# Kernel optimization log

Hardware: AMD Instinct MI355X
Metric: run time of the kernel (lower is better)

Reference implementation:

```python
import jax, jax.numpy as jnp
import numpy as np

N = 100000   # nodes
E = 1200000  # edges
IN, HID, OUT = 64, 64, 64
G = 64       # graphs in the batch


def setup_inputs() -> dict:
    key = jax.random.key(0)
    ks = jax.random.split(key, 7)
    x = jax.random.normal(ks[0], (N, IN), dtype=jnp.float32)
    edge_index = jax.random.randint(ks[1], (2, E), 0, N, dtype=jnp.int32)
    batch = jnp.sort(jax.random.randint(ks[2], (N,), 0, G, dtype=jnp.int32))
    W1 = jax.random.normal(ks[3], (IN, HID), dtype=jnp.float32) * (1.0 / np.sqrt(IN))
    b1 = jnp.zeros((HID,), dtype=jnp.float32)
    W2 = jax.random.normal(ks[4], (HID, OUT), dtype=jnp.float32) * (1.0 / np.sqrt(HID))
    b2 = jnp.zeros((OUT,), dtype=jnp.float32)
    return {"x": x, "edge_index": edge_index, "batch": batch,
            "W1": W1, "b1": b1, "W2": W2, "b2": b2}


def _gcn_conv(x, W, b, src, dst, dinv):
    # x' = D^{-1/2} (A + I) D^{-1/2} (x W) + b   (PyG GCNConv with self-loops)
    h = x @ W                                   # [N, F_out]
    norm = dinv[src] * dinv[dst]                # [E]
    agg = jax.ops.segment_sum(h[src] * norm[:, None], dst, num_segments=N)
    agg = agg + h * (dinv * dinv)[:, None]      # self-loop contribution
    return agg + b


def reference(x, edge_index, batch, W1, b1, W2, b2):
    src, dst = edge_index[0], edge_index[1]
    # degree with self-loops, counted at the aggregation target (PyG convention)
    deg = jax.ops.segment_sum(jnp.ones((E,), x.dtype), dst, num_segments=N) + 1.0
    dinv = jax.lax.rsqrt(deg)

    h1 = jax.nn.relu(_gcn_conv(x, W1, b1, src, dst, dinv))   # [N, HID]
    s1 = jax.ops.segment_sum(h1, batch, num_segments=G)      # [G, HID]
    h2 = jax.nn.relu(_gcn_conv(h1, W2, b2, src, dst, dinv))  # [N, OUT]
    s2 = jax.ops.segment_sum(h2, batch, num_segments=G)      # [G, OUT]
    return h2, jnp.concatenate([s1, s2], axis=1)
```

## Files before the change

kernel.cpp:

```cpp
#include <hip/hip_runtime.h>


#define FDIM 64
#define BSHIFT 7
#define MAXNB 1024
#define EBCAP 2048
#define COLCAP 3072
#define BCAP 4096

__device__ __forceinline__ unsigned short f2bf(float f) {
    union { float f; unsigned int u; } a; a.f = f;
    unsigned int u = a.u;
    unsigned int r = u + 0x7fffu + ((u >> 16) & 1u);
    return (unsigned short)(r >> 16);
}
__device__ __forceinline__ float bf2f(unsigned short s) {
    union { unsigned int u; float f; } a; a.u = ((unsigned int)s) << 16;
    return a.f;
}

__global__ __launch_bounds__(256, 4) void k_pre(
    const int* __restrict__ src, const int* __restrict__ dstp, int E,
    const int* __restrict__ batch, int N, int G, int gemmB, int scatB,
    const float* __restrict__ x, const float* __restrict__ W1,
    int* __restrict__ bucketFill, int* __restrict__ gstart,
    unsigned short* __restrict__ gb1, unsigned int* __restrict__ ebuf) {
    __shared__ __align__(16) char sm[33792];
    int tid = threadIdx.x;
    int bx = blockIdx.x;
    if (bx < gemmB) {
        float4* Ws = (float4*)sm;
        float (*Xs)[68] = (float(*)[68])(sm + 16384);
        ushort4* GB4 = (ushort4*)gb1;
        if (bx == 0 && tid < 16) GB4[(size_t)N * 16 + tid] = make_ushort4(0, 0, 0, 0);
        const float4* W4 = (const float4*)W1;
        for (int i = tid; i < 1024; i += 256) Ws[i] = W4[i];
        int rowBase = bx * 64;
        for (int i = tid; i < 1024; i += 256) {
            int r = i >> 4, f4 = i & 15;
            float4 v = make_float4(0.f, 0.f, 0.f, 0.f);
            if (rowBase + r < N) v = ((const float4*)x)[(size_t)(rowBase + r) * 16 + f4];
            *(float4*)&Xs[r][f4 * 4] = v;
        }
        __syncthreads();
        int r0 = (tid >> 4) * 4;
        int c4 = tid & 15;
        float4 acc0 = make_float4(0,0,0,0), acc1 = acc0, acc2 = acc0, acc3 = acc0;
#pragma unroll 16
        for (int k = 0; k < 64; k++) {
            float4 w = Ws[k * 16 + c4];
            float x0 = Xs[r0 + 0][k], x1 = Xs[r0 + 1][k], x2 = Xs[r0 + 2][k], x3 = Xs[r0 + 3][k];
            acc0.x += x0 * w.x; acc0.y += x0 * w.y; acc0.z += x0 * w.z; acc0.w += x0 * w.w;
            acc1.x += x1 * w.x; acc1.y += x1 * w.y; acc1.z += x1 * w.z; acc1.w += x1 * w.w;
            acc2.x += x2 * w.x; acc2.y += x2 * w.y; acc2.z += x2 * w.z; acc2.w += x2 * w.w;
            acc3.x += x3 * w.x; acc3.y += x3 * w.y; acc3.z += x3 * w.z; acc3.w += x3 * w.w;
        }
        float4 a[4] = {acc0, acc1, acc2, acc3};
#pragma unroll
        for (int i = 0; i < 4; i++) {
            int row = rowBase + r0 + i;
            if (row < N) {
                ushort4 pk;
                pk.x = f2bf(a[i].x); pk.y = f2bf(a[i].y);
                pk.z = f2bf(a[i].z); pk.w = f2bf(a[i].w);
                GB4[(size_t)row * 16 + c4] = pk;
            }
        }
        return;
    }
    if (bx < gemmB + scatB) {
        int* hist = (int*)sm;
        int* base = hist + MAXNB;
        for (int i = tid; i < MAXNB; i += 256) hist[i] = 0;
        __syncthreads();
        int e0 = (bx - gemmB) * 4096;
        int s[16], d[16], r[16];
#pragma unroll
        for (int k = 0; k < 16; k++) {
            int e = e0 + k * 256 + tid;
            bool valid = e < E;
            s[k] = valid ? src[e] : 0;
            d[k] = valid ? dstp[e] : 0;
            r[k] = valid ? atomicAdd(&hist[d[k] >> BSHIFT], 1) : 0;
        }
        __syncthreads();
        for (int i = tid; i < MAXNB; i += 256) {
            int c = hist[i];
            base[i] = c ? (i << 11) + atomicAdd(&bucketFill[i], c) : 0;
        }
        __syncthreads();
#pragma unroll
        for (int k = 0; k < 16; k++) {
            int e = e0 + k * 256 + tid;
            if (e < E)
                ebuf[base[d[k] >> BSHIFT] + r[k]] =
                    (unsigned int)s[k] | ((unsigned int)(d[k] & 127) << 17);
        }
        return;
    }
    int i = (bx - gemmB - scatB) * 256 + tid;
    if (i < N) {
        int b = batch[i];
        if (i == 0) { for (int g = 0; g <= b; g++) gstart[g] = 0; }
        else {
            int pp = batch[i - 1];
            for (int g = pp + 1; g <= b; g++) gstart[g] = i;
        }
        if (i == N - 1) { for (int g = b + 1; g <= G; g++) gstart[g] = N; }
    }
}

__global__ __launch_bounds__(256) void k_bsort(const unsigned int* __restrict__ ebuf,
                                               const int* __restrict__ bucketFill, int N,
                                               int* __restrict__ row_ptr,
                                               int* __restrict__ row_blocks,
                                               int* __restrict__ col,
                                               float* __restrict__ dinv,
                                               unsigned short* __restrict__ gb1) {
    __shared__ int cntL[128];
    __shared__ int scanL[128];
    __shared__ int fillL[128];
    __shared__ int colL[BCAP];
    __shared__ int padT;
    int b = blockIdx.x;
    int n0 = b << BSHIFT;
    int nCnt = N - n0; if (nCnt > 128) nCnt = 128;
    int t = threadIdx.x;
    if (b == 0 && t == 0) dinv[N] = 0.f;
    int cnt = bucketFill[b]; if (cnt > EBCAP) cnt = EBCAP;
    int lo = b << 11, hi = lo + cnt;
    int outBase = b * COLCAP;
    if (t < 128) { cntL[t] = 0; fillL[t] = 0; }
    __syncthreads();
    for (int e = lo + t; e < hi; e += 256)
        atomicAdd(&cntL[ebuf[e] >> 17], 1);
    __syncthreads();
    int pc = 0;
    if (t < 128) { pc = (cntL[t] + 7) & ~7; scanL[t] = pc; }
    __syncthreads();
    for (int off = 1; off < 128; off <<= 1) {
        int u = (t >= off && t < 128) ? scanL[t - off] : 0;
        __syncthreads();
        if (t < 128) scanL[t] += u;
        __syncthreads();
    }
    if (t == 127) padT = scanL[127];
    if (t < nCnt) {
        int ex = scanL[t] - pc;
        row_ptr[n0 + t] = outBase + ex;
        row_blocks[n0 + t] = pc >> 3;
        dinv[n0 + t] = rsqrtf((float)cntL[t] + 1.0f);
        scanL[t] = ex;
    }
    __syncthreads();
    int padTotal = padT;
    if (padTotal <= BCAP) {
        for (int i = t; i < padTotal; i += 256) colL[i] = N;
        __syncthreads();
        for (int e = lo + t; e < hi; e += 256) {
            unsigned int pr = ebuf[e];
            int d = pr >> 17;
            int r = scanL[d] + atomicAdd(&fillL[d], 1);
            colL[r] = (int)(pr & 0x1FFFFu);
        }
        __syncthreads();
        for (int i = t; i < padTotal; i += 256) col[outBase + i] = colL[i];
    } else {
        for (int e = lo + t; e < hi; e += 256) {
            unsigned int pr = ebuf[e];
            int d = pr >> 17;
            int r = scanL[d] + atomicAdd(&fillL[d], 1);
            col[outBase + r] = (int)(pr & 0x1FFFFu);
        }
        __syncthreads();
        if (t < nCnt) {
            int pcl = (cntL[t] + 7) & ~7;
            for (int i = cntL[t]; i < pcl; i++) col[outBase + scanL[t] + i] = N;
        }
    }
    __syncthreads();
    ushort4* GB4 = (ushort4*)gb1;
    for (int i = t; i < nCnt * 16; i += 256) {
        int row = i >> 4, u4 = i & 15;
        float dn = rsqrtf((float)cntL[row] + 1.0f);
        size_t idx = (size_t)(n0 + row) * 16 + u4;
        ushort4 u = GB4[idx];
        u.x = f2bf(bf2f(u.x) * dn);
        u.y = f2bf(bf2f(u.y) * dn);
        u.z = f2bf(bf2f(u.z) * dn);
        u.w = f2bf(bf2f(u.w) * dn);
        GB4[idx] = u;
    }
}

template <typename OutT>
__global__ __launch_bounds__(256) void k_agg(
    const unsigned short* __restrict__ Gb,
    const int* __restrict__ row_ptr, const int* __restrict__ row_blocks,
    const int* __restrict__ col, const float* __restrict__ dinv,
    const float* __restrict__ bias, int N, OutT* __restrict__ Out) {
    int w = threadIdx.x >> 6;
    int c = threadIdx.x & 63;
    int n = blockIdx.x * 4 + w;
    if (n >= N) return;
    int e = row_ptr[n];
    int nb8 = row_blocks[n];
    float acc = bf2f(Gb[(size_t)n * FDIM + c]);
    for (; nb8 >= 2; nb8 -= 2, e += 16) {
        int4 ca = *(const int4*)(col + e);
        int4 cb = *(const int4*)(col + e + 4);
        int4 cc = *(const int4*)(col + e + 8);
        int4 cd = *(const int4*)(col + e + 12);
        int s0  = __builtin_amdgcn_readfirstlane(ca.x);
        int s1  = __builtin_amdgcn_readfirstlane(ca.y);
        int s2  = __builtin_amdgcn_readfirstlane(ca.z);
        int s3  = __builtin_amdgcn_readfirstlane(ca.w);
        int s4  = __builtin_amdgcn_readfirstlane(cb.x);
        int s5  = __builtin_amdgcn_readfirstlane(cb.y);
        int s6  = __builtin_amdgcn_readfirstlane(cb.z);
        int s7  = __builtin_amdgcn_readfirstlane(cb.w);
        int s8  = __builtin_amdgcn_readfirstlane(cc.x);
        int s9  = __builtin_amdgcn_readfirstlane(cc.y);
        int s10 = __builtin_amdgcn_readfirstlane(cc.z);
        int s11 = __builtin_amdgcn_readfirstlane(cc.w);
        int s12 = __builtin_amdgcn_readfirstlane(cd.x);
        int s13 = __builtin_amdgcn_readfirstlane(cd.y);
        int s14 = __builtin_amdgcn_readfirstlane(cd.z);
        int s15 = __builtin_amdgcn_readfirstlane(cd.w);
        float a0  = bf2f(Gb[(size_t)s0  * FDIM + c]);
        float a1  = bf2f(Gb[(size_t)s1  * FDIM + c]);
        float a2  = bf2f(Gb[(size_t)s2  * FDIM + c]);
        float a3  = bf2f(Gb[(size_t)s3  * FDIM + c]);
        float a4  = bf2f(Gb[(size_t)s4  * FDIM + c]);
        float a5  = bf2f(Gb[(size_t)s5  * FDIM + c]);
        float a6  = bf2f(Gb[(size_t)s6  * FDIM + c]);
        float a7  = bf2f(Gb[(size_t)s7  * FDIM + c]);
        float a8  = bf2f(Gb[(size_t)s8  * FDIM + c]);
        float a9  = bf2f(Gb[(size_t)s9  * FDIM + c]);
        float a10 = bf2f(Gb[(size_t)s10 * FDIM + c]);
        float a11 = bf2f(Gb[(size_t)s11 * FDIM + c]);
        float a12 = bf2f(Gb[(size_t)s12 * FDIM + c]);
        float a13 = bf2f(Gb[(size_t)s13 * FDIM + c]);
        float a14 = bf2f(Gb[(size_t)s14 * FDIM + c]);
        float a15 = bf2f(Gb[(size_t)s15 * FDIM + c]);
        acc += (((a0 + a1) + (a2 + a3)) + ((a4 + a5) + (a6 + a7)))
             + (((a8 + a9) + (a10 + a11)) + ((a12 + a13) + (a14 + a15)));
    }
    if (nb8) {
        int4 ca = *(const int4*)(col + e);
        int4 cb = *(const int4*)(col + e + 4);
        int s0 = __builtin_amdgcn_readfirstlane(ca.x);
        int s1 = __builtin_amdgcn_readfirstlane(ca.y);
        int s2 = __builtin_amdgcn_readfirstlane(ca.z);
        int s3 = __builtin_amdgcn_readfirstlane(ca.w);
        int s4 = __builtin_amdgcn_readfirstlane(cb.x);
        int s5 = __builtin_amdgcn_readfirstlane(cb.y);
        int s6 = __builtin_amdgcn_readfirstlane(cb.z);
        int s7 = __builtin_amdgcn_readfirstlane(cb.w);
        float a0 = bf2f(Gb[(size_t)s0 * FDIM + c]);
        float a1 = bf2f(Gb[(size_t)s1 * FDIM + c]);
        float a2 = bf2f(Gb[(size_t)s2 * FDIM + c]);
        float a3 = bf2f(Gb[(size_t)s3 * FDIM + c]);
        float a4 = bf2f(Gb[(size_t)s4 * FDIM + c]);
        float a5 = bf2f(Gb[(size_t)s5 * FDIM + c]);
        float a6 = bf2f(Gb[(size_t)s6 * FDIM + c]);
        float a7 = bf2f(Gb[(size_t)s7 * FDIM + c]);
        acc += ((a0 + a1) + (a2 + a3)) + ((a4 + a5) + (a6 + a7));
    }
    float v = fmaxf(acc * dinv[n] + bias[c], 0.f);
    if constexpr (sizeof(OutT) == 2)
        Out[(size_t)n * FDIM + c] = f2bf(v);
    else
        Out[(size_t)n * FDIM + c] = v;
}

__global__ __launch_bounds__(256, 4) void k_gemm2(
    const unsigned short* __restrict__ H1b, const float* __restrict__ W2,
    const float* __restrict__ dinv, int N, unsigned short* __restrict__ Gb2) {
    __shared__ float4 Ws[64 * 16];
    __shared__ float Xs[64][68];
    int tid = threadIdx.x;
    ushort4* GB4 = (ushort4*)Gb2;
    if (blockIdx.x == 0 && tid < 16)
        GB4[(size_t)N * 16 + tid] = make_ushort4(0, 0, 0, 0);
    const float4* W4 = (const float4*)W2;
    for (int i = tid; i < 1024; i += 256) Ws[i] = W4[i];
    int rowBase = blockIdx.x * 64;
    const ushort4* H4 = (const ushort4*)H1b;
    for (int i = tid; i < 1024; i += 256) {
        int r = i >> 4, u4 = i & 15;
        float4 v = make_float4(0.f, 0.f, 0.f, 0.f);
        if (rowBase + r < N) {
            ushort4 u = H4[(size_t)(rowBase + r) * 16 + u4];
            v = make_float4(bf2f(u.x), bf2f(u.y), bf2f(u.z), bf2f(u.w));
        }
        *(float4*)&Xs[r][u4 * 4] = v;
    }
    __syncthreads();
    int r0 = (tid >> 4) * 4;
    int c4 = tid & 15;
    float4 acc0 = make_float4(0,0,0,0), acc1 = acc0, acc2 = acc0, acc3 = acc0;
#pragma unroll 16
    for (int k = 0; k < 64; k++) {
        float4 w = Ws[k * 16 + c4];
        float x0 = Xs[r0 + 0][k], x1 = Xs[r0 + 1][k], x2 = Xs[r0 + 2][k], x3 = Xs[r0 + 3][k];
        acc0.x += x0 * w.x; acc0.y += x0 * w.y; acc0.z += x0 * w.z; acc0.w += x0 * w.w;
        acc1.x += x1 * w.x; acc1.y += x1 * w.y; acc1.z += x1 * w.z; acc1.w += x1 * w.w;
        acc2.x += x2 * w.x; acc2.y += x2 * w.y; acc2.z += x2 * w.z; acc2.w += x2 * w.w;
        acc3.x += x3 * w.x; acc3.y += x3 * w.y; acc3.z += x3 * w.z; acc3.w += x3 * w.w;
    }
    float4 a[4] = {acc0, acc1, acc2, acc3};
#pragma unroll
    for (int i = 0; i < 4; i++) {
        int row = rowBase + r0 + i;
        if (row < N) {
            float dn = dinv[row];
            ushort4 pk;
            pk.x = f2bf(a[i].x * dn);
            pk.y = f2bf(a[i].y * dn);
            pk.z = f2bf(a[i].z * dn);
            pk.w = f2bf(a[i].w * dn);
            GB4[(size_t)row * 16 + c4] = pk;
        }
    }
}

__global__ __launch_bounds__(256) void k_pool(const unsigned short* __restrict__ H1b,
                                              const float4* __restrict__ H2,
                                              const int* __restrict__ gstart,
                                              float* __restrict__ pool) {
    int g = blockIdx.x & 63;
    int layer = blockIdx.x >> 6;
    int lo = gstart[g], hi = gstart[g + 1];
    int c4 = threadIdx.x & 15;
    int rl = threadIdx.x >> 4;
    float4 acc = make_float4(0.f, 0.f, 0.f, 0.f);
    if (layer == 0) {
        const ushort4* H = (const ushort4*)H1b;
        for (int r = lo + rl; r < hi; r += 16) {
            ushort4 u = H[(size_t)r * 16 + c4];
            acc.x += bf2f(u.x); acc.y += bf2f(u.y);
            acc.z += bf2f(u.z); acc.w += bf2f(u.w);
        }
    } else {
        for (int r = lo + rl; r < hi; r += 16) {
            float4 v = H2[(size_t)r * 16 + c4];
            acc.x += v.x; acc.y += v.y; acc.z += v.z; acc.w += v.w;
        }
    }
    __shared__ float4 sm[16][16];
    sm[rl][c4] = acc;
    __syncthreads();
    if (rl == 0) {
        float4 s = sm[0][c4];
#pragma unroll
        for (int k = 1; k < 16; k++) {
            float4 v = sm[k][c4];
            s.x += v.x; s.y += v.y; s.z += v.z; s.w += v.w;
        }
        float* dstq = &pool[(size_t)g * 128 + layer * 64 + c4 * 4];
        dstq[0] = s.x; dstq[1] = s.y; dstq[2] = s.z; dstq[3] = s.w;
    }
}

static inline size_t align256(size_t x) { return (x + 255) & ~(size_t)255; }

extern "C" void kernel_launch(void* const* d_in, const int* in_sizes, int n_in,
                              void* d_out, int out_size, void* d_ws, size_t ws_size,
                              hipStream_t stream) {
    const float* x     = (const float*)d_in[0];
    const int*   ei    = (const int*)d_in[1];
    const int*   batch = (const int*)d_in[2];
    const float* W1    = (const float*)d_in[3];
    const float* b1    = (const float*)d_in[4];
    const float* W2    = (const float*)d_in[5];
    const float* b2    = (const float*)d_in[6];

    const int N = in_sizes[0] / FDIM;
    const int E = in_sizes[1] / 2;
    const int G = 64;
    const int NB = (N + 127) >> BSHIFT;
    const int* src = ei;
    const int* dst = ei + E;

    char* p = (char*)d_ws;
    int* row_ptr     = (int*)p; p += align256(((size_t)N + 1) * 4);
    int* row_blocks  = (int*)p; p += align256((size_t)N * 4);
    int* col         = (int*)p; p += align256((size_t)NB * COLCAP * 4);
    int* bucketFill  = (int*)p; p += align256((size_t)MAXNB * 4);
    int* gstart      = (int*)p; p += align256((size_t)(G + 1) * 4);
    float* dinv      = (float*)p; p += align256(((size_t)N + 1) * 4);
    unsigned short* gb1 = (unsigned short*)p; p += align256(((size_t)N + 1) * FDIM * 2);
    unsigned short* gb2 = (unsigned short*)p; p += align256(((size_t)N + 1) * FDIM * 2);
    unsigned short* h1b = (unsigned short*)p; p += align256((size_t)N * FDIM * 2);
    unsigned int* ebuf = (unsigned int*)h1b;

    float* out  = (float*)d_out;
    float* h2   = out;
    float* pool = out + (size_t)N * FDIM;

    hipMemsetAsync(bucketFill, 0, (size_t)MAXNB * 4, stream);

    int nbB   = (N + 255) / 256;
    int gemmB = (N + 63) / 64;
    int aggB  = (N + 3) / 4;
    int scatB = (E + 4095) / 4096;

    k_pre<<<gemmB + scatB + nbB, 256, 0, stream>>>(src, dst, E, batch, N, G,
                                                   gemmB, scatB, x, W1,
                                                   bucketFill, gstart, gb1, ebuf);
    k_bsort<<<NB, 256, 0, stream>>>(ebuf, bucketFill, N, row_ptr, row_blocks,
                                    col, dinv, gb1);
    k_agg<unsigned short><<<aggB, 256, 0, stream>>>(gb1, row_ptr, row_blocks, col,
                                                    dinv, b1, N, h1b);
    k_gemm2<<<gemmB, 256, 0, stream>>>(h1b, W2, dinv, N, gb2);
    k_agg<float><<<aggB, 256, 0, stream>>>(gb2, row_ptr, row_blocks, col,
                                           dinv, b2, N, h2);
    k_pool<<<2 * G, 256, 0, stream>>>(h1b, (const float4*)h2, gstart, pool);
}
```

Before: 244.2 us.

## Fuse graph pooling into gemm2 and agg2, move dinv scaling into agg1

Removes the separate pooling kernel and the gstart computation. Layer-1 pooling now runs inside k_gemm2 over its staged H1 tile, and layer-2 pooling runs inside the second aggregation, both with per-graph running sums and atomicAdd after zeroing pool with a memset. The pass in k_bsort that rescaled gb1 by dinv is dropped. Instead the first aggregation multiplies each gathered neighbour by dinv[src], which adds 16 scalar gathers per edge block in exchange for one fewer read-modify-write of gb1. It adds atomic traffic and a block-level sync in the aggregation kernel.

```diff
diff --git a/kernel.cpp b/kernel.cpp
--- a/kernel.cpp
+++ b/kernel.cpp
@@ -21,9 +21,9 @@
 
 __global__ __launch_bounds__(256, 4) void k_pre(
     const int* __restrict__ src, const int* __restrict__ dstp, int E,
-    const int* __restrict__ batch, int N, int G, int gemmB, int scatB,
+    int N, int gemmB,
     const float* __restrict__ x, const float* __restrict__ W1,
-    int* __restrict__ bucketFill, int* __restrict__ gstart,
+    int* __restrict__ bucketFill,
     unsigned short* __restrict__ gb1, unsigned int* __restrict__ ebuf) {
     __shared__ __align__(16) char sm[33792];
     int tid = threadIdx.x;
@@ -68,45 +68,32 @@
         }
         return;
     }
-    if (bx < gemmB + scatB) {
-        int* hist = (int*)sm;
-        int* base = hist + MAXNB;
-        for (int i = tid; i < MAXNB; i += 256) hist[i] = 0;
-        __syncthreads();
-        int e0 = (bx - gemmB) * 4096;
-        int s[16], d[16], r[16];
+    int* hist = (int*)sm;
+    int* base = hist + MAXNB;
+    for (int i = tid; i < MAXNB; i += 256) hist[i] = 0;
+    __syncthreads();
+    int e0 = (bx - gemmB) * 4096;
+    int s[16], d[16], r[16];
 #pragma unroll
-        for (int k = 0; k < 16; k++) {
-            int e = e0 + k * 256 + tid;
-            bool valid = e < E;
-            s[k] = valid ? src[e] : 0;
-            d[k] = valid ? dstp[e] : 0;
-            r[k] = valid ? atomicAdd(&hist[d[k] >> BSHIFT], 1) : 0;
-        }
-        __syncthreads();
-        for (int i = tid; i < MAXNB; i += 256) {
-            int c = hist[i];
-            base[i] = c ? (i << 11) + atomicAdd(&bucketFill[i], c) : 0;
-        }
-        __syncthreads();
+    for (int k = 0; k < 16; k++) {
+        int e = e0 + k * 256 + tid;
+        bool valid = e < E;
+        s[k] = valid ? src[e] : 0;
+        d[k] = valid ? dstp[e] : 0;
+        r[k] = valid ? atomicAdd(&hist[d[k] >> BSHIFT], 1) : 0;
+    }
+    __syncthreads();
+    for (int i = tid; i < MAXNB; i += 256) {
+        int c = hist[i];
+        base[i] = c ? (i << 11) + atomicAdd(&bucketFill[i], c) : 0;
+    }
+    __syncthreads();
 #pragma unroll
-        for (int k = 0; k < 16; k++) {
-            int e = e0 + k * 256 + tid;
-            if (e < E)
-                ebuf[base[d[k] >> BSHIFT] + r[k]] =
-                    (unsigned int)s[k] | ((unsigned int)(d[k] & 127) << 17);
-        }
-        return;
-    }
-    int i = (bx - gemmB - scatB) * 256 + tid;
-    if (i < N) {
-        int b = batch[i];
-        if (i == 0) { for (int g = 0; g <= b; g++) gstart[g] = 0; }
-        else {
-            int pp = batch[i - 1];
-            for (int g = pp + 1; g <= b; g++) gstart[g] = i;
-        }
-        if (i == N - 1) { for (int g = b + 1; g <= G; g++) gstart[g] = N; }
+    for (int k = 0; k < 16; k++) {
+        int e = e0 + k * 256 + tid;
+        if (e < E)
+            ebuf[base[d[k] >> BSHIFT] + r[k]] =
+                (unsigned int)s[k] | ((unsigned int)(d[k] & 127) << 17);
     }
 }
 
@@ -115,8 +102,7 @@
                                                int* __restrict__ row_ptr,
                                                int* __restrict__ row_blocks,
                                                int* __restrict__ col,
-                                               float* __restrict__ dinv,
-                                               unsigned short* __restrict__ gb1) {
+                                               float* __restrict__ dinv) {
     __shared__ int cntL[128];
     __shared__ int scanL[128];
     __shared__ int fillL[128];
@@ -178,34 +164,28 @@
             for (int i = cntL[t]; i < pcl; i++) col[outBase + scanL[t] + i] = N;
         }
     }
-    __syncthreads();
-    ushort4* GB4 = (ushort4*)gb1;
-    for (int i = t; i < nCnt * 16; i += 256) {
-        int row = i >> 4, u4 = i & 15;
-        float dn = rsqrtf((float)cntL[row] + 1.0f);
-        size_t idx = (size_t)(n0 + row) * 16 + u4;
-        ushort4 u = GB4[idx];
-        u.x = f2bf(bf2f(u.x) * dn);
-        u.y = f2bf(bf2f(u.y) * dn);
-        u.z = f2bf(bf2f(u.z) * dn);
-        u.w = f2bf(bf2f(u.w) * dn);
-        GB4[idx] = u;
-    }
-}
-
-template <typename OutT>
+}
+
+template <typename OutT, bool EDGE_DINV, bool POOL>
 __global__ __launch_bounds__(256) void k_agg(
     const unsigned short* __restrict__ Gb,
     const int* __restrict__ row_ptr, const int* __restrict__ row_blocks,
     const int* __restrict__ col, const float* __restrict__ dinv,
-    const float* __restrict__ bias, int N, OutT* __restrict__ Out) {
+    const float* __restrict__ bias, const int* __restrict__ batch,
+    int N, OutT* __restrict__ Out, float* __restrict__ pool) {
     int w = threadIdx.x >> 6;
     int c = threadIdx.x & 63;
     int n = blockIdx.x * 4 + w;
-    if (n >= N) return;
-    int e = row_ptr[n];
-    int nb8 = row_blocks[n];
-    float acc = bf2f(Gb[(size_t)n * FDIM + c]);
+    bool alive = n < N;
+    int e = 0, nb8 = 0;
+    float acc = 0.f, dn = 0.f;
+    if (alive) {
+        e = row_ptr[n];
+        nb8 = row_blocks[n];
+        dn = dinv[n];
+        float self = bf2f(Gb[(size_t)n * FDIM + c]);
+        acc = EDGE_DINV ? self * dn : self;
+    }
     for (; nb8 >= 2; nb8 -= 2, e += 16) {
         int4 ca = *(const int4*)(col + e);
         int4 cb = *(const int4*)(col + e + 4);
@@ -243,8 +223,17 @@
         float a13 = bf2f(Gb[(size_t)s13 * FDIM + c]);
         float a14 = bf2f(Gb[(size_t)s14 * FDIM + c]);
         float a15 = bf2f(Gb[(size_t)s15 * FDIM + c]);
-        acc += (((a0 + a1) + (a2 + a3)) + ((a4 + a5) + (a6 + a7)))
-             + (((a8 + a9) + (a10 + a11)) + ((a12 + a13) + (a14 + a15)));
+        if constexpr (EDGE_DINV) {
+            float d0  = dinv[s0],  d1  = dinv[s1],  d2  = dinv[s2],  d3  = dinv[s3];
+            float d4  = dinv[s4],  d5  = dinv[s5],  d6  = dinv[s6],  d7  = dinv[s7];
+            float d8  = dinv[s8],  d9  = dinv[s9],  d10 = dinv[s10], d11 = dinv[s11];
+            float d12 = dinv[s12], d13 = dinv[s13], d14 = dinv[s14], d15 = dinv[s15];
+            acc += (((a0*d0 + a1*d1) + (a2*d2 + a3*d3)) + ((a4*d4 + a5*d5) + (a6*d6 + a7*d7)))
+                 + (((a8*d8 + a9*d9) + (a10*d10 + a11*d11)) + ((a12*d12 + a13*d13) + (a14*d14 + a15*d15)));
+        } else {
+            acc += (((a0 + a1) + (a2 + a3)) + ((a4 + a5) + (a6 + a7)))
+                 + (((a8 + a9) + (a10 + a11)) + ((a12 + a13) + (a14 + a15)));
+        }
     }
     if (nb8) {
         int4 ca = *(const int4*)(col + e);
@@ -265,20 +254,51 @@
         float a5 = bf2f(Gb[(size_t)s5 * FDIM + c]);
         float a6 = bf2f(Gb[(size_t)s6 * FDIM + c]);
         float a7 = bf2f(Gb[(size_t)s7 * FDIM + c]);
-        acc += ((a0 + a1) + (a2 + a3)) + ((a4 + a5) + (a6 + a7));
-    }
-    float v = fmaxf(acc * dinv[n] + bias[c], 0.f);
-    if constexpr (sizeof(OutT) == 2)
-        Out[(size_t)n * FDIM + c] = f2bf(v);
-    else
-        Out[(size_t)n * FDIM + c] = v;
+        if constexpr (EDGE_DINV) {
+            float d0 = dinv[s0], d1 = dinv[s1], d2 = dinv[s2], d3 = dinv[s3];
+            float d4 = dinv[s4], d5 = dinv[s5], d6 = dinv[s6], d7 = dinv[s7];
+            acc += ((a0*d0 + a1*d1) + (a2*d2 + a3*d3)) + ((a4*d4 + a5*d5) + (a6*d6 + a7*d7));
+        } else {
+            acc += ((a0 + a1) + (a2 + a3)) + ((a4 + a5) + (a6 + a7));
+        }
+    }
+    float v = 0.f;
+    if (alive) {
+        v = fmaxf(acc * dn + bias[c], 0.f);
+        if constexpr (sizeof(OutT) == 2)
+            Out[(size_t)n * FDIM + c] = f2bf(v);
+        else
+            Out[(size_t)n * FDIM + c] = v;
+    }
+    if constexpr (POOL) {
+        __shared__ float smv[4][64];
+        __shared__ int gsm[4];
+        smv[w][c] = v;
+        if (c == 0) gsm[w] = alive ? batch[n] : -1;
+        __syncthreads();
+        if (w == 0) {
+            float run = 0.f; int gcur = -2;
+#pragma unroll
+            for (int i = 0; i < 4; i++) {
+                int g = gsm[i];
+                if (g != gcur) {
+                    if (gcur >= 0) atomicAdd(&pool[(size_t)gcur * 128 + 64 + c], run);
+                    run = 0.f; gcur = g;
+                }
+                run += smv[i][c];
+            }
+            if (gcur >= 0) atomicAdd(&pool[(size_t)gcur * 128 + 64 + c], run);
+        }
+    }
 }
 
 __global__ __launch_bounds__(256, 4) void k_gemm2(
     const unsigned short* __restrict__ H1b, const float* __restrict__ W2,
-    const float* __restrict__ dinv, int N, unsigned short* __restrict__ Gb2) {
+    const float* __restrict__ dinv, const int* __restrict__ batch, int N,
+    unsigned short* __restrict__ Gb2, float* __restrict__ pool) {
     __shared__ float4 Ws[64 * 16];
     __shared__ float Xs[64][68];
+    __shared__ int bsL[64];
     int tid = threadIdx.x;
     ushort4* GB4 = (ushort4*)Gb2;
     if (blockIdx.x == 0 && tid < 16)
@@ -286,6 +306,10 @@
     const float4* W4 = (const float4*)W2;
     for (int i = tid; i < 1024; i += 256) Ws[i] = W4[i];
     int rowBase = blockIdx.x * 64;
+    if (tid < 64) {
+        int row = rowBase + tid;
+        bsL[tid] = (row < N) ? batch[row] : -1;
+    }
     const ushort4* H4 = (const ushort4*)H1b;
     for (int i = tid; i < 1024; i += 256) {
         int r = i >> 4, u4 = i & 15;
@@ -323,43 +347,21 @@
             GB4[(size_t)row * 16 + c4] = pk;
         }
     }
-}
-
-__global__ __launch_bounds__(256) void k_pool(const unsigned short* __restrict__ H1b,
-                                              const float4* __restrict__ H2,
-                                              const int* __restrict__ gstart,
-                                              float* __restrict__ pool) {
-    int g = blockIdx.x & 63;
-    int layer = blockIdx.x >> 6;
-    int lo = gstart[g], hi = gstart[g + 1];
-    int c4 = threadIdx.x & 15;
-    int rl = threadIdx.x >> 4;
-    float4 acc = make_float4(0.f, 0.f, 0.f, 0.f);
-    if (layer == 0) {
-        const ushort4* H = (const ushort4*)H1b;
-        for (int r = lo + rl; r < hi; r += 16) {
-            ushort4 u = H[(size_t)r * 16 + c4];
-            acc.x += bf2f(u.x); acc.y += bf2f(u.y);
-            acc.z += bf2f(u.z); acc.w += bf2f(u.w);
-        }
-    } else {
-        for (int r = lo + rl; r < hi; r += 16) {
-            float4 v = H2[(size_t)r * 16 + c4];
-            acc.x += v.x; acc.y += v.y; acc.z += v.z; acc.w += v.w;
-        }
-    }
-    __shared__ float4 sm[16][16];
-    sm[rl][c4] = acc;
-    __syncthreads();
-    if (rl == 0) {
-        float4 s = sm[0][c4];
-#pragma unroll
-        for (int k = 1; k < 16; k++) {
-            float4 v = sm[k][c4];
-            s.x += v.x; s.y += v.y; s.z += v.z; s.w += v.w;
-        }
-        float* dstq = &pool[(size_t)g * 128 + layer * 64 + c4 * 4];
-        dstq[0] = s.x; dstq[1] = s.y; dstq[2] = s.z; dstq[3] = s.w;
+    {
+        int cc = tid & 63;
+        int seg = tid >> 6;
+        float run = 0.f; int gcur = -2;
+        for (int rl = 0; rl < 16; rl++) {
+            int r = seg * 16 + rl;
+            int g = bsL[r];
+            if (g < 0) break;
+            if (g != gcur) {
+                if (gcur >= 0) atomicAdd(&pool[(size_t)gcur * 128 + cc], run);
+                run = 0.f; gcur = g;
+            }
+            run += Xs[r][cc];
+        }
+        if (gcur >= 0) atomicAdd(&pool[(size_t)gcur * 128 + cc], run);
     }
 }
 
@@ -388,7 +390,6 @@
     int* row_blocks  = (int*)p; p += align256((size_t)N * 4);
     int* col         = (int*)p; p += align256((size_t)NB * COLCAP * 4);
     int* bucketFill  = (int*)p; p += align256((size_t)MAXNB * 4);
-    int* gstart      = (int*)p; p += align256((size_t)(G + 1) * 4);
     float* dinv      = (float*)p; p += align256(((size_t)N + 1) * 4);
     unsigned short* gb1 = (unsigned short*)p; p += align256(((size_t)N + 1) * FDIM * 2);
     unsigned short* gb2 = (unsigned short*)p; p += align256(((size_t)N + 1) * FDIM * 2);
@@ -400,21 +401,19 @@
     float* pool = out + (size_t)N * FDIM;
 
     hipMemsetAsync(bucketFill, 0, (size_t)MAXNB * 4, stream);
-
-    int nbB   = (N + 255) / 256;
+    hipMemsetAsync(pool, 0, (size_t)G * 128 * 4, stream);
+
     int gemmB = (N + 63) / 64;
     int aggB  = (N + 3) / 4;
     int scatB = (E + 4095) / 4096;
 
-    k_pre<<<gemmB + scatB + nbB, 256, 0, stream>>>(src, dst, E, batch, N, G,
-                                                   gemmB, scatB, x, W1,
-                                                   bucketFill, gstart, gb1, ebuf);
+    k_pre<<<gemmB + scatB, 256, 0, stream>>>(src, dst, E, N, gemmB, x, W1,
+                                             bucketFill, gb1, ebuf);
     k_bsort<<<NB, 256, 0, stream>>>(ebuf, bucketFill, N, row_ptr, row_blocks,
-                                    col, dinv, gb1);
-    k_agg<unsigned short><<<aggB, 256, 0, stream>>>(gb1, row_ptr, row_blocks, col,
-                                                    dinv, b1, N, h1b);
-    k_gemm2<<<gemmB, 256, 0, stream>>>(h1b, W2, dinv, N, gb2);
-    k_agg<float><<<aggB, 256, 0, stream>>>(gb2, row_ptr, row_blocks, col,
-                                           dinv, b2, N, h2);
-    k_pool<<<2 * G, 256, 0, stream>>>(h1b, (const float4*)h2, gstart, pool);
-}
+                                    col, dinv);
+    k_agg<unsigned short, true, false><<<aggB, 256, 0, stream>>>(
+        gb1, row_ptr, row_blocks, col, dinv, b1, nullptr, N, h1b, nullptr);
+    k_gemm2<<<gemmB, 256, 0, stream>>>(h1b, W2, dinv, batch, N, gb2, pool);
+    k_agg<float, false, true><<<aggB, 256, 0, stream>>>(
+        gb2, row_ptr, row_blocks, col, dinv, b2, batch, N, h2, pool);
+}
```

Result: slower. 254.0 us (+4.0%).
